# Kernel optimization log

Measured on AMD Instinct MI355X. Metric: run time of the kernel, lower is better.

## Reference

```python
import jax, jax.numpy as jnp
import numpy as np

RFF_DIM = 256
ATTENTION_SCALE = 0.1
LAMBDA_REG = 0.01
SIGMA = 1.0


def setup_inputs() -> dict:
    key = jax.random.key(0)
    k1, k2, k3 = jax.random.split(key, 3)
    N, D_IN = 262144, 64
    Z = jax.random.normal(k1, (N, D_IN), dtype=jnp.float32)
    W_rff = jax.random.normal(k2, (D_IN, RFF_DIM), dtype=jnp.float32)
    A = jax.random.normal(k3, (2 * RFF_DIM, 3), dtype=jnp.float32) * 0.01
    return {"Z": Z, "W_rff": W_rff, "A": A}


def reference(Z, W_rff, A):
    # --- RFF transform: Q = sqrt(1/R) * [cos(Z W / sigma), sin(Z W / sigma)] ---
    proj = (Z @ W_rff) / SIGMA                       # [N, R]
    Q = jnp.sqrt(1.0 / RFF_DIM) * jnp.concatenate(
        [jnp.cos(proj), jnp.sin(proj)], axis=-1)      # [N, 2R]

    N, F = Q.shape
    chunk = max(F // RFF_DIM, 1)                      # = 2 here
    n_chunks = F // chunk                             # = RFF_DIM

    # --- convexified attention over feature chunks (vectorized) ---
    Qc = Q.reshape(N, n_chunks, chunk)                # [N, K, c]
    A_mean = jnp.mean(A, axis=-1)                     # [2R]
    # per-chunk trace score: mean over batch of <Q_i, A_mean[:c]>
    scores = jnp.mean(jnp.einsum('nkc,c->nk', Qc, A_mean[:chunk]), axis=0)  # [K]
    alpha = jax.nn.softmax(scores / (ATTENTION_SCALE * np.sqrt(RFF_DIM)))   # [K]
    # per-chunk reweighting (dim-preserving recombination)
    Q_tilde = (alpha[None, :, None] * Qc).reshape(N, F)                      # [N, 2R]

    # --- small GEMM head + nuclear-norm regularizer ---
    predictions = Q_tilde @ A                          # [N, out]
    AW = jax.nn.softmax(predictions / np.sqrt(RFF_DIM), axis=-1)
    nuclear_norm = jnp.sum(jnp.linalg.svd(A, compute_uv=False))
    reg_loss = LAMBDA_REG * nuclear_norm
    return predictions, AW, reg_loss, alpha
```

## Files before the change

### kernel.cpp

```cpp
#include <hip/hip_runtime.h>
#include <math.h>

#define N_ROWS 262144
#define D_IN 64
#define RFF 256
#define NTILES (N_ROWS / 16)
#define GRID 1024

#define OFF_PRED 0
#define OFF_AW (N_ROWS * 3)
#define OFF_REG (2 * N_ROWS * 3)
#define OFF_ALPHA (2 * N_ROWS * 3 + 1)

#define WS_B 512
#define WS_WF 1280

typedef _Float16 f16x8 __attribute__((ext_vector_type(8)));
typedef float f32x4 __attribute__((ext_vector_type(4)));
typedef float f32x2 __attribute__((ext_vector_type(2)));

__device__ __forceinline__ f32x4 mfma16(f16x8 a, f16x8 b, f32x4 c) {
    return __builtin_amdgcn_mfma_f32_16x16x32_f16(a, b, c, 0, 0, 0);
}

__device__ __forceinline__ unsigned short f32_to_bf16_rne(float x) {
    unsigned int u = __float_as_uint(x);
    unsigned int r = u + 0x7fffu + ((u >> 16) & 1u);
    return (unsigned short)(r >> 16);
}

__device__ __forceinline__ void sincos_rev(float pr, float& sn, float& cs) {
    float f;
    asm("v_fract_f32 %0, %1" : "=v"(f) : "v"(pr));
    asm("v_sin_f32 %0, %1" : "=v"(sn) : "v"(f));
    asm("v_cos_f32 %0, %1" : "=v"(cs) : "v"(f));
}

__device__ __forceinline__ float rowsum16(float x) {
    x += __int_as_float(__builtin_amdgcn_mov_dpp(__float_as_int(x), 0x121, 0xf, 0xf, true));
    x += __int_as_float(__builtin_amdgcn_mov_dpp(__float_as_int(x), 0x122, 0xf, 0xf, true));
    x += __int_as_float(__builtin_amdgcn_mov_dpp(__float_as_int(x), 0x124, 0xf, 0xf, true));
    x += __int_as_float(__builtin_amdgcn_mov_dpp(__float_as_int(x), 0x128, 0xf, 0xf, true));
    return x;
}

__device__ __forceinline__ void gload_lds16(const float* g, float* lds) {
    __builtin_amdgcn_global_load_lds(
        (const __attribute__((address_space(1))) unsigned int*)g,
        (__attribute__((address_space(3))) unsigned int*)(lds), 16, 0, 0);
}

#define WAITVM0() do { asm volatile("s_waitcnt vmcnt(0)" ::: "memory"); \
                       __builtin_amdgcn_sched_barrier(0); } while (0)
#define WAITVM1() do { asm volatile("s_waitcnt vmcnt(1)" ::: "memory"); \
                       __builtin_amdgcn_sched_barrier(0); } while (0)
#define LGKM0()   do { asm volatile("s_waitcnt lgkmcnt(0)" ::: "memory"); \
                       __builtin_amdgcn_sched_barrier(0); } while (0)

__global__ __launch_bounds__(256) void k_prep(const float* __restrict__ W,
                                              float* __restrict__ ws) {
    const int e = blockIdx.x * 256 + threadIdx.x;
    if (e < 512) ws[e] = 0.f;
    const int lane = e & 63;
    const int slot = e >> 6;
    const int kh = slot & 1;
    const int ct = slot >> 1;
    const int k0 = kh * 32 + 8 * (lane >> 4);
    const int col = ct * 16 + (lane & 15);
    f16x8 v;
#pragma unroll
    for (int i = 0; i < 8; ++i)
        v[i] = (_Float16)(W[(k0 + i) * RFF + col] * 0.15915494309189535f);
    *(f16x8*)(ws + WS_WF + e * 4) = v;
}

__device__ __forceinline__ void dma_Bf_half(const float* __restrict__ wsWf, float* Bf,
                                            int h, int wv, int l) {
#pragma unroll
    for (int m = 0; m < 4; ++m) {
        const int off = wv * 1024 + m * 256;
        gload_lds16(wsWf + h * 4096 + off + l * 4, Bf + off);
    }
}

__device__ __forceinline__ void stage_dma(const float* __restrict__ Z, int n0, int l,
                                          float* ldsbase) {
#pragma unroll
    for (int m = 0; m < 4; ++m) {
        const int row = m * 4 + (l >> 4);
        const int gc = (l & 15) ^ (row & 7);
        gload_lds16(Z + (size_t)(n0 + row) * D_IN + gc * 4, ldsbase + m * 256);
    }
}

__device__ __forceinline__ void frags_from_lds(const float* bb, int lr, int lh,
                                               f16x8& ah0, f16x8& ah1) {
    const int s4 = lr & 7;
    const float* rp = bb + lr * 64;
    float z[16];
    *(float4*)&z[0]  = *(const float4*)(rp + (((lh * 2 + 0) ^ s4) << 2));
    *(float4*)&z[4]  = *(const float4*)(rp + (((lh * 2 + 1) ^ s4) << 2));
    *(float4*)&z[8]  = *(const float4*)(rp + (((lh * 2 + 8) ^ s4) << 2));
    *(float4*)&z[12] = *(const float4*)(rp + (((lh * 2 + 9) ^ s4) << 2));
    LGKM0();
#pragma unroll
    for (int i = 0; i < 8; ++i) {
        ah0[i] = (_Float16)z[i];
        ah1[i] = (_Float16)z[8 + i];
    }
}

__global__ __launch_bounds__(256, 4) void k_pass1(const float* __restrict__ Z,
                                                  const float* __restrict__ ws_in,
                                                  float* __restrict__ U) {
    __shared__ float Bff[4096];
    __shared__ float Zs[4][1024];
    __shared__ float Ured[256];
    const int t = threadIdx.x;
    const int wv = t >> 6, l = t & 63, lr = l & 15, lh = l >> 4;
    const int h = blockIdx.x & 1;
    const int g = blockIdx.x >> 1;

    dma_Bf_half(ws_in + WS_WF, Bff, h, wv, l);
    const int tstart = g * 32 + wv * 8;
    stage_dma(Z, tstart * 16, l, &Zs[wv][0]);
    Ured[t] = 0.f;
    __syncthreads();

    const f16x8* Bf = (const f16x8*)Bff;
    f32x2 accC2[8], accS2[8];
#pragma unroll
    for (int c = 0; c < 8; ++c) { accC2[c] = (f32x2){0.f, 0.f}; accS2[c] = (f32x2){0.f, 0.f}; }

    for (int tt = 0; tt < 8; ++tt) {
        if (tt) WAITVM0();
        f16x8 ah0, ah1;
        frags_from_lds(&Zs[wv][0], lr, lh, ah0, ah1);
        if (tt + 1 < 8) {
            stage_dma(Z, (tstart + tt + 1) * 16, l, &Zs[wv][0]);
            __builtin_amdgcn_sched_barrier(0);
        }
        f32x4 acc[8];
#pragma unroll
        for (int c = 0; c < 8; ++c) acc[c] = (f32x4){0.f, 0.f, 0.f, 0.f};
#pragma unroll
        for (int c = 0; c < 8; ++c) {
            acc[c] = mfma16(ah0, Bf[(c * 2 + 0) * 64 + l], acc[c]);
            acc[c] = mfma16(ah1, Bf[(c * 2 + 1) * 64 + l], acc[c]);
        }
#pragma unroll
        for (int c = 0; c < 8; ++c) {
            float sn0, cs0, sn1, cs1, sn2, cs2, sn3, cs3;
            sincos_rev(acc[c][0], sn0, cs0);
            sincos_rev(acc[c][1], sn1, cs1);
            sincos_rev(acc[c][2], sn2, cs2);
            sincos_rev(acc[c][3], sn3, cs3);
            accC2[c] += (f32x2){cs0, cs1};
            accC2[c] += (f32x2){cs2, cs3};
            accS2[c] += (f32x2){sn0, sn1};
            accS2[c] += (f32x2){sn2, sn3};
        }
    }
#pragma unroll
    for (int c = 0; c < 8; ++c) {
        float cc = accC2[c][0] + accC2[c][1];
        float ss = accS2[c][0] + accS2[c][1];
        cc += __shfl_xor(cc, 16);
        cc += __shfl_xor(cc, 32);
        ss += __shfl_xor(ss, 16);
        ss += __shfl_xor(ss, 32);
        if (l < 16) {
            atomicAdd(&Ured[c * 16 + l], cc * 0.0625f);
            atomicAdd(&Ured[128 + c * 16 + l], ss * 0.0625f);
        }
    }
    __syncthreads();
    if (t < 128) atomicAdd(&U[128 * h + t], Ured[t]);
    else atomicAdd(&U[256 + 128 * h + (t - 128)], Ured[t]);
}

__global__ __launch_bounds__(256) void k_alpha(const float* __restrict__ U,
                                               const float* __restrict__ A,
                                               float* __restrict__ ws,
                                               float* __restrict__ out) {
    __shared__ float sm[256];
    __shared__ double gred[256];
    __shared__ double G6[6];
    const int k = threadIdx.x;

    const float am0 = (A[0] + A[1] + A[2]) * (1.0f / 3.0f);
    const float am1 = (A[3] + A[4] + A[5]) * (1.0f / 3.0f);
    float x = (am0 * U[2 * k] + am1 * U[2 * k + 1]) * (1.0f / (float)N_ROWS) * (1.0f / 1.6f);

    sm[k] = x;
    __syncthreads();
    for (int s = 128; s > 0; s >>= 1) {
        if (k < s) sm[k] = fmaxf(sm[k], sm[k + s]);
        __syncthreads();
    }
    float mx = sm[0];
    __syncthreads();
    float e = __expf(x - mx);
    sm[k] = e;
    __syncthreads();
    for (int s = 128; s > 0; s >>= 1) {
        if (k < s) sm[k] += sm[k + s];
        __syncthreads();
    }
    float al = e / sm[0];
    out[OFF_ALPHA + k] = al;
    sm[k] = al;
    __syncthreads();

    {
        const float ac = 0.0625f * sm[k >> 1];
        const float as = 0.0625f * sm[128 + (k >> 1)];
        unsigned int* BtP = (unsigned int*)(ws + WS_B);
        const int dst = (k >> 7) * 384 + (k & 127) * 3;
#pragma unroll
        for (int j = 0; j < 3; ++j) {
            float bc = ac * A[k * 3 + j];
            float bs = as * A[(256 + k) * 3 + j];
            unsigned int ulo = f32_to_bf16_rne(bc);
            unsigned int uhi = f32_to_bf16_rne(bs);
            BtP[dst + j] = ulo | (uhi << 16);
        }
    }

    double af[2][3];
#pragma unroll
    for (int t2 = 0; t2 < 2; ++t2)
#pragma unroll
        for (int j = 0; j < 3; ++j) af[t2][j] = (double)A[(k + t2 * 256) * 3 + j];
    const int ei[6] = {0, 0, 0, 1, 1, 2};
    const int ej[6] = {0, 1, 2, 1, 2, 2};
    for (int eidx = 0; eidx < 6; ++eidx) {
        double p = af[0][ei[eidx]] * af[0][ej[eidx]] + af[1][ei[eidx]] * af[1][ej[eidx]];
        gred[k] = p;
        __syncthreads();
        for (int s = 128; s > 0; s >>= 1) {
            if (k < s) gred[k] += gred[k + s];
            __syncthreads();
        }
        if (k == 0) G6[eidx] = gred[0];
        __syncthreads();
    }
    if (k == 0) {
        double g00 = G6[0], g01 = G6[1], g02 = G6[2], g11 = G6[3], g12 = G6[4], g22 = G6[5];
        double q = (g00 + g11 + g22) / 3.0;
        double p1 = g01 * g01 + g02 * g02 + g12 * g12;
        double p2 = (g00 - q) * (g00 - q) + (g11 - q) * (g11 - q) + (g22 - q) * (g22 - q) + 2.0 * p1;
        double nuc;
        if (p2 < 1e-300) {
            nuc = 3.0 * sqrt(fmax(q, 0.0));
        } else {
            double p = sqrt(p2 / 6.0);
            double b00 = (g00 - q) / p, b11 = (g11 - q) / p, b22 = (g22 - q) / p;
            double b01 = g01 / p, b02 = g02 / p, b12 = g12 / p;
            double detB = b00 * (b11 * b22 - b12 * b12) - b01 * (b01 * b22 - b12 * b02) +
                          b02 * (b01 * b12 - b11 * b02);
            double rr = fmin(1.0, fmax(-1.0, detB / 2.0));
            double phi = acos(rr) / 3.0;
            double e1 = q + 2.0 * p * cos(phi);
            double e3 = q + 2.0 * p * cos(phi + 2.0943951023931953);
            double e2 = 3.0 * q - e1 - e3;
            nuc = sqrt(fmax(e1, 0.0)) + sqrt(fmax(e2, 0.0)) + sqrt(fmax(e3, 0.0));
        }
        out[OFF_REG] = (float)(0.01 * nuc);
    }
}

__global__ __launch_bounds__(256, 4) void k_pass2(const float* __restrict__ Z,
                                                  const float* __restrict__ ws_in,
                                                  float* __restrict__ out) {
    __shared__ float Bff[4096];
    __shared__ float Zs[4][1024];
    __shared__ unsigned int BtP[384];
    const int t = threadIdx.x;
    const int wv = t >> 6, l = t & 63, lr = l & 15, lh = l >> 4;
    const int h = blockIdx.x & 1;
    const int g = blockIdx.x >> 1;

    dma_Bf_half(ws_in + WS_WF, Bff, h, wv, l);
    const int tstart = g * 32 + wv * 8;
    stage_dma(Z, tstart * 16, l, &Zs[wv][0]);
    {
        const unsigned int* src = (const unsigned int*)(ws_in + WS_B) + h * 384;
        BtP[t] = src[t];
        if (t < 128) BtP[256 + t] = src[256 + t];
    }
    __syncthreads();

    const f16x8* Bf = (const f16x8*)Bff;
    const size_t ob = h ? (size_t)OFF_AW : (size_t)OFF_PRED;

    for (int tt = 0; tt < 8; ++tt) {
        const int n0 = (tstart + tt) * 16;
        if (tt) WAITVM1();
        f16x8 ah0, ah1;
        frags_from_lds(&Zs[wv][0], lr, lh, ah0, ah1);
        if (tt + 1 < 8) {
            stage_dma(Z, (tstart + tt + 1) * 16, l, &Zs[wv][0]);
            __builtin_amdgcn_sched_barrier(0);
        }
        f32x4 acc[8];
#pragma unroll
        for (int c = 0; c < 8; ++c) acc[c] = (f32x4){0.f, 0.f, 0.f, 0.f};
#pragma unroll
        for (int c = 0; c < 8; ++c) {
            acc[c] = mfma16(ah0, Bf[(c * 2 + 0) * 64 + l], acc[c]);
            acc[c] = mfma16(ah1, Bf[(c * 2 + 1) * 64 + l], acc[c]);
        }
        f32x2 pa01[3], pa23[3];
#pragma unroll
        for (int j = 0; j < 3; ++j) { pa01[j] = (f32x2){0.f, 0.f}; pa23[j] = (f32x2){0.f, 0.f}; }
#pragma unroll
        for (int c = 0; c < 8; ++c) {
            const int fl = c * 16 + lr;
            unsigned int u0 = BtP[fl * 3 + 0], u1 = BtP[fl * 3 + 1], u2 = BtP[fl * 3 + 2];
            float sn0, cs0, sn1, cs1, sn2, cs2, sn3, cs3;
            sincos_rev(acc[c][0], sn0, cs0);
            sincos_rev(acc[c][1], sn1, cs1);
            sincos_rev(acc[c][2], sn2, cs2);
            sincos_rev(acc[c][3], sn3, cs3);
            const f32x2 cs01 = {cs0, cs1}, cs23 = {cs2, cs3};
            const f32x2 sn01 = {sn0, sn1}, sn23 = {sn2, sn3};
            const float bcf[3] = {__uint_as_float(u0 << 16), __uint_as_float(u1 << 16),
                                  __uint_as_float(u2 << 16)};
            const float bsf[3] = {__uint_as_float(u0 & 0xffff0000u),
                                  __uint_as_float(u1 & 0xffff0000u),
                                  __uint_as_float(u2 & 0xffff0000u)};
#pragma unroll
            for (int j = 0; j < 3; ++j) {
                const f32x2 bc2 = {bcf[j], bcf[j]};
                const f32x2 bs2 = {bsf[j], bsf[j]};
                pa01[j] = __builtin_elementwise_fma(
                    cs01, bc2, __builtin_elementwise_fma(sn01, bs2, pa01[j]));
                pa23[j] = __builtin_elementwise_fma(
                    cs23, bc2, __builtin_elementwise_fma(sn23, bs2, pa23[j]));
            }
        }
        float pa[4][3];
#pragma unroll
        for (int j = 0; j < 3; ++j) {
            pa[0][j] = rowsum16(pa01[j][0]);
            pa[1][j] = rowsum16(pa01[j][1]);
            pa[2][j] = rowsum16(pa23[j][0]);
            pa[3][j] = rowsum16(pa23[j][1]);
        }
        float val = 0.f;
#pragma unroll
        for (int r = 0; r < 4; ++r)
#pragma unroll
            for (int j = 0; j < 3; ++j)
                if (lr == r * 3 + j) val = pa[r][j];
        if (lr < 12) {
            out[ob + ((size_t)n0 + 4 * lh) * 3 + lr] = val;
        }
    }
}

__global__ __launch_bounds__(256) void k_aw(float* __restrict__ out) {
    const size_t n = (size_t)blockIdx.x * 256 + threadIdx.x;
    const float a0 = out[OFF_PRED + n * 3 + 0], b0 = out[OFF_AW + n * 3 + 0];
    const float a1 = out[OFF_PRED + n * 3 + 1], b1 = out[OFF_AW + n * 3 + 1];
    const float a2 = out[OFF_PRED + n * 3 + 2], b2 = out[OFF_AW + n * 3 + 2];
    const float p0 = a0 + b0, p1 = a1 + b1, p2 = a2 + b2;
    out[OFF_PRED + n * 3 + 0] = p0;
    out[OFF_PRED + n * 3 + 1] = p1;
    out[OFF_PRED + n * 3 + 2] = p2;
    const float x0 = p0 * 0.0625f, x1 = p1 * 0.0625f, x2 = p2 * 0.0625f;
    const float m = fmaxf(x0, fmaxf(x1, x2));
    const float e0 = __expf(x0 - m), e1 = __expf(x1 - m), e2 = __expf(x2 - m);
    const float inv = 1.0f / (e0 + e1 + e2);
    out[OFF_AW + n * 3 + 0] = e0 * inv;
    out[OFF_AW + n * 3 + 1] = e1 * inv;
    out[OFF_AW + n * 3 + 2] = e2 * inv;
}

extern "C" void kernel_launch(void* const* d_in, const int* in_sizes, int n_in,
                              void* d_out, int out_size, void* d_ws, size_t ws_size,
                              hipStream_t stream) {
    const float* Z = (const float*)d_in[0];
    const float* W = (const float*)d_in[1];
    const float* A = (const float*)d_in[2];
    float* out = (float*)d_out;
    float* ws = (float*)d_ws;

    hipLaunchKernelGGL(k_prep, dim3(8), dim3(256), 0, stream, W, ws);
    hipLaunchKernelGGL(k_pass1, dim3(GRID), dim3(256), 0, stream, Z, ws, ws);
    hipLaunchKernelGGL(k_alpha, dim3(1), dim3(256), 0, stream, ws, A, ws, out);
    hipLaunchKernelGGL(k_pass2, dim3(GRID), dim3(256), 0, stream, Z, ws, out);
    hipLaunchKernelGGL(k_aw, dim3(N_ROWS / 256), dim3(256), 0, stream, out);
}
```

Measured before the change: 86.50 us.

## Hold W_rff fragments in registers, interleave MFMA with sincos, remap block order

```diff
diff --git a/kernel.cpp b/kernel.cpp
--- a/kernel.cpp
+++ b/kernel.cpp
@@ -74,15 +74,6 @@
     *(f16x8*)(ws + WS_WF + e * 4) = v;
 }
 
-__device__ __forceinline__ void dma_Bf_half(const float* __restrict__ wsWf, float* Bf,
-                                            int h, int wv, int l) {
-#pragma unroll
-    for (int m = 0; m < 4; ++m) {
-        const int off = wv * 1024 + m * 256;
-        gload_lds16(wsWf + h * 4096 + off + l * 4, Bf + off);
-    }
-}
-
 __device__ __forceinline__ void stage_dma(const float* __restrict__ Z, int n0, int l,
                                           float* ldsbase) {
 #pragma unroll
@@ -113,21 +104,24 @@
 __global__ __launch_bounds__(256, 4) void k_pass1(const float* __restrict__ Z,
                                                   const float* __restrict__ ws_in,
                                                   float* __restrict__ U) {
-    __shared__ float Bff[4096];
     __shared__ float Zs[4][1024];
     __shared__ float Ured[256];
     const int t = threadIdx.x;
     const int wv = t >> 6, l = t & 63, lr = l & 15, lh = l >> 4;
-    const int h = blockIdx.x & 1;
-    const int g = blockIdx.x >> 1;
-
-    dma_Bf_half(ws_in + WS_WF, Bff, h, wv, l);
+    const int nb = (blockIdx.x & 7) * 128 + (blockIdx.x >> 3);
+    const int h = nb & 1;
+    const int g = nb >> 1;
+
+    const float* wsWf = ws_in + WS_WF + h * 4096;
+    f16x8 B[16];
+#pragma unroll
+    for (int s = 0; s < 16; ++s) B[s] = *(const f16x8*)(wsWf + s * 256 + l * 4);
+
     const int tstart = g * 32 + wv * 8;
     stage_dma(Z, tstart * 16, l, &Zs[wv][0]);
     Ured[t] = 0.f;
     __syncthreads();
 
-    const f16x8* Bf = (const f16x8*)Bff;
     f32x2 accC2[8], accS2[8];
 #pragma unroll
     for (int c = 0; c < 8; ++c) { accC2[c] = (f32x2){0.f, 0.f}; accS2[c] = (f32x2){0.f, 0.f}; }
@@ -140,21 +134,16 @@
             stage_dma(Z, (tstart + tt + 1) * 16, l, &Zs[wv][0]);
             __builtin_amdgcn_sched_barrier(0);
         }
-        f32x4 acc[8];
-#pragma unroll
-        for (int c = 0; c < 8; ++c) acc[c] = (f32x4){0.f, 0.f, 0.f, 0.f};
 #pragma unroll
         for (int c = 0; c < 8; ++c) {
-            acc[c] = mfma16(ah0, Bf[(c * 2 + 0) * 64 + l], acc[c]);
-            acc[c] = mfma16(ah1, Bf[(c * 2 + 1) * 64 + l], acc[c]);
-        }
-#pragma unroll
-        for (int c = 0; c < 8; ++c) {
+            f32x4 acc = (f32x4){0.f, 0.f, 0.f, 0.f};
+            acc = mfma16(ah0, B[c * 2 + 0], acc);
+            acc = mfma16(ah1, B[c * 2 + 1], acc);
             float sn0, cs0, sn1, cs1, sn2, cs2, sn3, cs3;
-            sincos_rev(acc[c][0], sn0, cs0);
-            sincos_rev(acc[c][1], sn1, cs1);
-            sincos_rev(acc[c][2], sn2, cs2);
-            sincos_rev(acc[c][3], sn3, cs3);
+            sincos_rev(acc[0], sn0, cs0);
+            sincos_rev(acc[1], sn1, cs1);
+            sincos_rev(acc[2], sn2, cs2);
+            sincos_rev(acc[3], sn3, cs3);
             accC2[c] += (f32x2){cs0, cs1};
             accC2[c] += (f32x2){cs2, cs3};
             accS2[c] += (f32x2){sn0, sn1};
@@ -273,15 +262,19 @@
 __global__ __launch_bounds__(256, 4) void k_pass2(const float* __restrict__ Z,
                                                   const float* __restrict__ ws_in,
                                                   float* __restrict__ out) {
-    __shared__ float Bff[4096];
     __shared__ float Zs[4][1024];
     __shared__ unsigned int BtP[384];
     const int t = threadIdx.x;
     const int wv = t >> 6, l = t & 63, lr = l & 15, lh = l >> 4;
-    const int h = blockIdx.x & 1;
-    const int g = blockIdx.x >> 1;
-
-    dma_Bf_half(ws_in + WS_WF, Bff, h, wv, l);
+    const int nb = (blockIdx.x & 7) * 128 + (blockIdx.x >> 3);
+    const int h = nb & 1;
+    const int g = nb >> 1;
+
+    const float* wsWf = ws_in + WS_WF + h * 4096;
+    f16x8 B[16];
+#pragma unroll
+    for (int s = 0; s < 16; ++s) B[s] = *(const f16x8*)(wsWf + s * 256 + l * 4);
+
     const int tstart = g * 32 + wv * 8;
     stage_dma(Z, tstart * 16, l, &Zs[wv][0]);
     {
@@ -291,7 +284,6 @@
     }
     __syncthreads();
 
-    const f16x8* Bf = (const f16x8*)Bff;
     const size_t ob = h ? (size_t)OFF_AW : (size_t)OFF_PRED;
 
     for (int tt = 0; tt < 8; ++tt) {
@@ -303,26 +295,21 @@
             stage_dma(Z, (tstart + tt + 1) * 16, l, &Zs[wv][0]);
             __builtin_amdgcn_sched_barrier(0);
         }
-        f32x4 acc[8];
-#pragma unroll
-        for (int c = 0; c < 8; ++c) acc[c] = (f32x4){0.f, 0.f, 0.f, 0.f};
+        f32x2 pa01[3], pa23[3];
+#pragma unroll
+        for (int j = 0; j < 3; ++j) { pa01[j] = (f32x2){0.f, 0.f}; pa23[j] = (f32x2){0.f, 0.f}; }
 #pragma unroll
         for (int c = 0; c < 8; ++c) {
-            acc[c] = mfma16(ah0, Bf[(c * 2 + 0) * 64 + l], acc[c]);
-            acc[c] = mfma16(ah1, Bf[(c * 2 + 1) * 64 + l], acc[c]);
-        }
-        f32x2 pa01[3], pa23[3];
-#pragma unroll
-        for (int j = 0; j < 3; ++j) { pa01[j] = (f32x2){0.f, 0.f}; pa23[j] = (f32x2){0.f, 0.f}; }
-#pragma unroll
-        for (int c = 0; c < 8; ++c) {
+            f32x4 acc = (f32x4){0.f, 0.f, 0.f, 0.f};
+            acc = mfma16(ah0, B[c * 2 + 0], acc);
+            acc = mfma16(ah1, B[c * 2 + 1], acc);
             const int fl = c * 16 + lr;
             unsigned int u0 = BtP[fl * 3 + 0], u1 = BtP[fl * 3 + 1], u2 = BtP[fl * 3 + 2];
             float sn0, cs0, sn1, cs1, sn2, cs2, sn3, cs3;
-            sincos_rev(acc[c][0], sn0, cs0);
-            sincos_rev(acc[c][1], sn1, cs1);
-            sincos_rev(acc[c][2], sn2, cs2);
-            sincos_rev(acc[c][3], sn3, cs3);
+            sincos_rev(acc[0], sn0, cs0);
+            sincos_rev(acc[1], sn1, cs1);
+            sincos_rev(acc[2], sn2, cs2);
+            sincos_rev(acc[3], sn3, cs3);
             const f32x2 cs01 = {cs0, cs1}, cs23 = {cs2, cs3};
             const f32x2 sn01 = {sn0, sn1}, sn23 = {sn2, sn3};
             const float bcf[3] = {__uint_as_float(u0 << 16), __uint_as_float(u1 << 16),
```

After: 81.92 us. -5.3%, faster.
